# Kernel tuning notes

Measured on AMD Instinct MI355X. Metric: run time of the kernel, lower is better.

The kernel has to match this reference:

```python
import jax, jax.numpy as jnp
import numpy as np

N_INTERP = 5      # `count = 5` in the original
MAXDIS = 0.001    # threshold default (thresholding/list-build is data-dependent; see notes)


def _pairwise_edge_cdis(recon, gt):
    """Fused, vectorized version of the original double Python loop.

    recon: [B, N, D] keypoints; gt: [B, M, D].
    Returns cdis [B, P] where P = N*(N-1)/2 lower-triangular pairs (i>j),
    cdis[b, p] = mean over 5 interpolated points of min squared distance to gt[b].
    """
    B, N, D = recon.shape
    ii, jj = jnp.tril_indices(N, -1)                 # P pairs, i > j (same order as the loops)
    P = ii.shape[0]
    start = recon[:, ii, :]                          # [B, P, D]
    end = recon[:, jj, :]                            # [B, P, D]
    f = jnp.linspace(0.0, 1.0, N_INTERP, dtype=recon.dtype).reshape(1, 1, N_INTERP, 1)
    # K = start * f_interp + end * (1 - f_interp)   -> [B, P, 5, D]
    K = start[:, :, None, :] * f + end[:, :, None, :] * (1.0 - f)
    Kf = K.reshape(B, P * N_INTERP, D)               # flatten pairs x interp
    diff = Kf[:, :, None, :] - gt[:, None, :, :]     # [B, P*5, M, D]
    dist = jnp.sum(diff * diff, axis=3)              # [B, P*5, M] squared distances
    dmin = jnp.min(dist, axis=2)                     # min over gt points (dist1 in original)
    cdis = jnp.mean(dmin.reshape(B, P, N_INTERP), axis=2)  # mean over 5 interp points
    return cdis                                      # [B, P]


def setup_inputs() -> dict:
    key = jax.random.key(0)
    k1, k2 = jax.random.split(key)
    return {
        "recon_points": jax.random.uniform(k1, (4, 64, 3), dtype=jnp.float32),
        "gt_points": jax.random.uniform(k2, (4, 2048, 3), dtype=jnp.float32),
    }


def reference(recon_points, gt_points):
    # Dense, fixed-shape equivalent of compute_edge_distance: the per-(batch, pair)
    # chamfer distance. The original thresholds cdis < maxdis and builds a python
    # dict of edges; that is a trivial host-side post-process of this tensor.
    return _pairwise_edge_cdis(recon_points, gt_points)
```

## Files before the change

### kernel.cpp

```cpp
#include <hip/hip_runtime.h>
#include <hip/hip_bf16.h>
#include <math.h>

#define BATCH 4
#define NPTS 64
#define MGT 2048
#define NPAIR 2016
#define PPW 4
#define THREADS 512
#define WAVES_PER_BLOCK 8
#define CHUNKS_PER_BLOCK WAVES_PER_BLOCK
#define BLOCKS_PER_BATCH 63

__global__ __launch_bounds__(THREADS)
void edge_cdis_kernel(const float* __restrict__ recon,
                      const float* __restrict__ gt,
                      float* __restrict__ out) {
    __shared__ float4 gts4[MGT];

    const int tid  = threadIdx.x;
    const int wib  = tid >> 6;
    const int lane = tid & 63;

    const int b  = blockIdx.x / BLOCKS_PER_BATCH;
    const int cb = (blockIdx.x % BLOCKS_PER_BATCH) * CHUNKS_PER_BLOCK + wib;

    const float* __restrict__ gtb = gt + b * (MGT * 3);
    #pragma unroll
    for (int p = tid; p < MGT; p += THREADS) {
        const float gx = gtb[p * 3 + 0];
        const float gy = gtb[p * 3 + 1];
        const float gz = gtb[p * 3 + 2];
        float4 v;
        v.x = -gx; v.y = -gy; v.z = -gz;
        v.w = 0.5f * fmaf(gz, gz, fmaf(gy, gy, gx * gx));
        gts4[p] = v;
    }
    __syncthreads();

    int i_[PPW], j_[PPW];
    if (cb >= 496) {
        const int base = (cb - 496) * 4;
        #pragma unroll
        for (int k = 0; k < PPW; ++k) { i_[k] = 32; j_[k] = base + k; }
    } else {
        const int P = cb >> 4;
        const int o = cb & 15;
        const int a = P + 1;
        const int bb = 63 - P;
        const int slot = o * 4;
        #pragma unroll
        for (int k = 0; k < PPW; ++k) {
            const int sk = slot + k;
            i_[k] = (sk < a) ? a : bb;
            j_[k] = (sk < a) ? sk : (sk - a);
        }
    }
    const bool same_row = (i_[0] == i_[PPW - 1]);

    const float* __restrict__ rb = recon + b * (NPTS * 3);

    float ex[PPW], ey[PPW], ez[PPW];
    float sx[PPW], sy[PPW], sz[PPW];
    float cadd[PPW];
    #pragma unroll
    for (int k = 0; k < PPW; ++k) {
        sx[k] = rb[i_[k] * 3 + 0]; sy[k] = rb[i_[k] * 3 + 1]; sz[k] = rb[i_[k] * 3 + 2];
        ex[k] = rb[j_[k] * 3 + 0]; ey[k] = rb[j_[k] * 3 + 1]; ez[k] = rb[j_[k] * 3 + 2];
        const float ux = sx[k] - ex[k], uy = sy[k] - ey[k], uz = sz[k] - ez[k];
        const float e2 = ex[k]*ex[k] + ey[k]*ey[k] + ez[k]*ez[k];
        const float eu = ex[k]*ux + ey[k]*uy + ez[k]*uz;
        const float c  = ux*ux + uy*uy + uz*uz;
        cadd[k] = e2 + eu + 0.375f * c;
    }

    float r[PPW][5];
    #pragma unroll
    for (int k = 0; k < PPW; ++k)
        #pragma unroll
        for (int t = 0; t < 5; ++t) r[k][t] = 3.4e38f;
    float r4s = 3.4e38f;

    if (same_row) {
        const float Sx = sx[0], Sy = sy[0], Sz = sz[0];
        #pragma unroll 4
        for (int g = lane; g < MGT; g += 64) {
            const float4 gv = gts4[g];
            float Ds = fmaf(Sx, gv.x, gv.w);
            Ds = fmaf(Sy, gv.y, Ds);
            Ds = fmaf(Sz, gv.z, Ds);
            r4s = fminf(r4s, Ds);
            #pragma unroll
            for (int k = 0; k < PPW; ++k) {
                float A = fmaf(ex[k], gv.x, gv.w);
                A = fmaf(ey[k], gv.y, A);
                A = fmaf(ez[k], gv.z, A);
                const float G = Ds - A;
                r[k][0] = fminf(r[k][0], A);
                r[k][1] = fminf(r[k][1], fmaf(0.25f, G, A));
                r[k][2] = fminf(r[k][2], fmaf(0.50f, G, A));
                r[k][3] = fminf(r[k][3], fmaf(0.75f, G, A));
            }
        }
    } else {
        #pragma unroll 4
        for (int g = lane; g < MGT; g += 64) {
            const float4 gv = gts4[g];
            #pragma unroll
            for (int k = 0; k < PPW; ++k) {
                float A = fmaf(ex[k], gv.x, gv.w);
                A = fmaf(ey[k], gv.y, A);
                A = fmaf(ez[k], gv.z, A);
                float Ds = fmaf(sx[k], gv.x, gv.w);
                Ds = fmaf(sy[k], gv.y, Ds);
                Ds = fmaf(sz[k], gv.z, Ds);
                const float G = Ds - A;
                r[k][0] = fminf(r[k][0], A);
                r[k][1] = fminf(r[k][1], fmaf(0.25f, G, A));
                r[k][2] = fminf(r[k][2], fmaf(0.50f, G, A));
                r[k][3] = fminf(r[k][3], fmaf(0.75f, G, A));
                r[k][4] = fminf(r[k][4], Ds);
            }
        }
    }

    #pragma unroll
    for (int k = 0; k < PPW; ++k)
        #pragma unroll
        for (int t = 0; t < 5; ++t)
            #pragma unroll
            for (int off = 32; off >= 1; off >>= 1)
                r[k][t] = fminf(r[k][t], __shfl_xor(r[k][t], off, 64));
    #pragma unroll
    for (int off = 32; off >= 1; off >>= 1)
        r4s = fminf(r4s, __shfl_xor(r4s, off, 64));

    if (lane == 0) {
        #pragma unroll
        for (int k = 0; k < PPW; ++k) {
            const float r4 = same_row ? r4s : r[k][4];
            const float sr = r[k][0] + r[k][1] + r[k][2] + r[k][3] + r4;
            const int p = i_[k] * (i_[k] - 1) / 2 + j_[k];
            out[b * NPAIR + p] = 0.4f * sr + cadd[k];
        }
    }
}

extern "C" void kernel_launch(void* const* d_in, const int* in_sizes, int n_in,
                              void* d_out, int out_size, void* d_ws, size_t ws_size,
                              hipStream_t stream) {
    const float* recon = (const float*)d_in[0];
    const float* gt    = (const float*)d_in[1];
    float* out = (float*)d_out;

    const int blocks = BATCH * BLOCKS_PER_BATCH;
    edge_cdis_kernel<<<blocks, THREADS, 0, stream>>>(recon, gt, out);
}
```

Measured before the change: 14.92 us.

## Halve pairs per wave, double block size, use linear pair indexing

```diff
diff --git a/kernel.cpp b/kernel.cpp
--- a/kernel.cpp
+++ b/kernel.cpp
@@ -6,10 +6,10 @@
 #define NPTS 64
 #define MGT 2048
 #define NPAIR 2016
-#define PPW 4
-#define THREADS 512
-#define WAVES_PER_BLOCK 8
-#define CHUNKS_PER_BLOCK WAVES_PER_BLOCK
+#define PPW 2
+#define THREADS 1024
+#define WAVES_PER_BLOCK 16
+#define CHUNKS_PER_BLOCK 16
 #define BLOCKS_PER_BATCH 63
 
 __global__ __launch_bounds__(THREADS)
@@ -36,30 +36,18 @@
         v.w = 0.5f * fmaf(gz, gz, fmaf(gy, gy, gx * gx));
         gts4[p] = v;
     }
-    __syncthreads();
 
-    int i_[PPW], j_[PPW];
-    if (cb >= 496) {
-        const int base = (cb - 496) * 4;
-        #pragma unroll
-        for (int k = 0; k < PPW; ++k) { i_[k] = 32; j_[k] = base + k; }
-    } else {
-        const int P = cb >> 4;
-        const int o = cb & 15;
-        const int a = P + 1;
-        const int bb = 63 - P;
-        const int slot = o * 4;
-        #pragma unroll
-        for (int k = 0; k < PPW; ++k) {
-            const int sk = slot + k;
-            i_[k] = (sk < a) ? a : bb;
-            j_[k] = (sk < a) ? sk : (sk - a);
-        }
-    }
-    const bool same_row = (i_[0] == i_[PPW - 1]);
+    const int p0 = 2 * cb;
+    int i0 = (int)((1.0f + sqrtf(1.0f + 8.0f * (float)p0)) * 0.5f);
+    while (i0 * (i0 - 1) / 2 > p0) --i0;
+    while ((i0 + 1) * i0 / 2 <= p0) ++i0;
+    const int j0 = p0 - i0 * (i0 - 1) / 2;
+    const bool same_row = (j0 + 1 < i0);
+    const int i1 = same_row ? i0 : (i0 + 1);
+    const int j1 = same_row ? (j0 + 1) : 0;
 
     const float* __restrict__ rb = recon + b * (NPTS * 3);
-
+    int i_[PPW] = {i0, i1}, j_[PPW] = {j0, j1};
     float ex[PPW], ey[PPW], ez[PPW];
     float sx[PPW], sy[PPW], sz[PPW];
     float cadd[PPW];
@@ -74,6 +62,8 @@
         cadd[k] = e2 + eu + 0.375f * c;
     }
 
+    __syncthreads();
+
     float r[PPW][5];
     #pragma unroll
     for (int k = 0; k < PPW; ++k)
@@ -83,7 +73,7 @@
 
     if (same_row) {
         const float Sx = sx[0], Sy = sy[0], Sz = sz[0];
-        #pragma unroll 4
+        #pragma unroll 8
         for (int g = lane; g < MGT; g += 64) {
             const float4 gv = gts4[g];
             float Ds = fmaf(Sx, gv.x, gv.w);
@@ -103,7 +93,7 @@
             }
         }
     } else {
-        #pragma unroll 4
+        #pragma unroll 8
         for (int g = lane; g < MGT; g += 64) {
             const float4 gv = gts4[g];
             #pragma unroll
@@ -127,21 +117,28 @@
     #pragma unroll
     for (int k = 0; k < PPW; ++k)
         #pragma unroll
-        for (int t = 0; t < 5; ++t)
+        for (int t = 0; t < 4; ++t)
             #pragma unroll
             for (int off = 32; off >= 1; off >>= 1)
                 r[k][t] = fminf(r[k][t], __shfl_xor(r[k][t], off, 64));
-    #pragma unroll
-    for (int off = 32; off >= 1; off >>= 1)
-        r4s = fminf(r4s, __shfl_xor(r4s, off, 64));
+    if (same_row) {
+        #pragma unroll
+        for (int off = 32; off >= 1; off >>= 1)
+            r4s = fminf(r4s, __shfl_xor(r4s, off, 64));
+    } else {
+        #pragma unroll
+        for (int k = 0; k < PPW; ++k)
+            #pragma unroll
+            for (int off = 32; off >= 1; off >>= 1)
+                r[k][4] = fminf(r[k][4], __shfl_xor(r[k][4], off, 64));
+    }
 
     if (lane == 0) {
         #pragma unroll
         for (int k = 0; k < PPW; ++k) {
             const float r4 = same_row ? r4s : r[k][4];
             const float sr = r[k][0] + r[k][1] + r[k][2] + r[k][3] + r4;
-            const int p = i_[k] * (i_[k] - 1) / 2 + j_[k];
-            out[b * NPAIR + p] = 0.4f * sr + cadd[k];
+            out[b * NPAIR + p0 + k] = 0.4f * sr + cadd[k];
         }
     }
 }
```

Result: faster. 12.67 us (-15.1%).
